# Kernel tuning notes

Measured on AMD Instinct MI355X. Metric: run time of the kernel, lower is better.

The kernel has to match this reference:

```python
import jax, jax.numpy as jnp
import numpy as np
import math


def setup_inputs() -> dict:
    key = jax.random.key(0)
    k1, k2 = jax.random.split(key)
    B, C, H, W = 16, 128, 56, 56
    Cw, ks = 16, 3  # grouped dynamic weights: groups = C // Cw = 8
    x = jax.random.normal(k1, (B, C, H, W), dtype=jnp.float32)
    w = jax.random.normal(k2, (B, Cw, ks * ks, H, W), dtype=jnp.float32)
    return {"x": x, "w": w}


def reference(x, w):
    # x: [B, C, H, W]; w: [B, Cw, ks*ks, H, W] (5-D path of SKA.forward)
    B, C, H, W = x.shape
    ks_sq = w.shape[2]
    ks = int(math.isqrt(ks_sq))
    pad = (ks - 1) // 2
    Cw = w.shape[1]
    if Cw != C:
        # torch w.repeat(1, groups, 1, 1, 1) tiles along the channel dim
        w = jnp.tile(w, (1, C // Cw, 1, 1, 1))
    # Fused equivalent of unfold * w -> sum over kernel taps: accumulate
    # shifted views of the padded input weighted by per-pixel kernels.
    xp = jnp.pad(x, ((0, 0), (0, 0), (pad, pad), (pad, pad)))
    out = jnp.zeros_like(x)
    for i in range(ks):
        for j in range(ks):
            # F.unfold flattens taps row-major: k = i * ks + j
            out = out + xp[:, :, i:i + H, j:j + W] * w[:, :, i * ks + j]
    return out
```

## Files before the change

kernel.cpp:

```cpp
#include <hip/hip_runtime.h>


#define SKA_B   16
#define SKA_C   128
#define SKA_CW  16
#define SKA_H   56
#define SKA_W   56
#define SKA_HW  (SKA_H * SKA_W)
#define SKA_G   (SKA_C / SKA_CW)

__global__ __launch_bounds__(256) void ska_kernel(
    const float* __restrict__ x,
    const float* __restrict__ w,
    float* __restrict__ out)
{
    const int tid = blockIdx.x * blockDim.x + threadIdx.x;
    const int hw  = tid % SKA_HW;
    const int bcw = tid / SKA_HW;
    const int cw  = bcw % SKA_CW;
    const int b   = bcw / SKA_CW;
    if (b >= SKA_B) return;

    const int h  = hw / SKA_W;
    const int ww = hw - h * SKA_W;

    const float* wp = w + ((size_t)(b * SKA_CW + cw) * 9) * SKA_HW + hw;
    float wk[9];
#pragma unroll
    for (int k = 0; k < 9; ++k) wk[k] = wp[(size_t)k * SKA_HW];

    const bool hv0 = (h - 1) >= 0;
    const bool hv2 = (h + 1) < SKA_H;
    const bool wv0 = (ww - 1) >= 0;
    const bool wv2 = (ww + 1) < SKA_W;

    const float* xb = x   + ((size_t)b * SKA_C + cw) * SKA_HW;
    float*       ob = out + ((size_t)b * SKA_C + cw) * SKA_HW + hw;

#pragma unroll
    for (int g = 0; g < SKA_G; ++g) {
        const float* xc = xb + (size_t)g * SKA_CW * SKA_HW + hw;
        float acc = 0.0f;

        if (hv0) {
            if (wv0) acc += xc[-SKA_W - 1] * wk[0];
                     acc += xc[-SKA_W    ] * wk[1];
            if (wv2) acc += xc[-SKA_W + 1] * wk[2];
        }
        {
            if (wv0) acc += xc[-1] * wk[3];
                     acc += xc[ 0] * wk[4];
            if (wv2) acc += xc[ 1] * wk[5];
        }
        if (hv2) {
            if (wv0) acc += xc[SKA_W - 1] * wk[6];
                     acc += xc[SKA_W    ] * wk[7];
            if (wv2) acc += xc[SKA_W + 1] * wk[8];
        }

        ob[(size_t)g * SKA_CW * SKA_HW] = acc;
    }
}

extern "C" void kernel_launch(void* const* d_in, const int* in_sizes, int n_in,
                              void* d_out, int out_size, void* d_ws, size_t ws_size,
                              hipStream_t stream) {
    const float* x = (const float*)d_in[0];
    const float* w = (const float*)d_in[1];
    float* out = (float*)d_out;

    const int total_threads = SKA_B * SKA_CW * SKA_HW;
    const int block = 256;
    const int grid = (total_threads + block - 1) / block;

    ska_kernel<<<grid, block, 0, stream>>>(x, w, out);
}
```

Before: 128.7 us.

## Compute four adjacent output columns per thread with float4 loads and stores

Each thread now produces four consecutive output pixels in a row. Weights, input rows and outputs move through 128-bit float4 accesses, and horizontally neighbouring input values are shared across the four outputs instead of being loaded again. This is meant to cut the number of memory instructions and redundant loads in a memory-bound stencil. In exchange the grid shrinks by four times and each thread uses more registers, and the row boundaries need scalar edge loads. The grid size relies on the total thread count dividing evenly by 256, and it does (200704 threads = 784 blocks).

```diff
diff --git a/kernel.cpp b/kernel.cpp
--- a/kernel.cpp
+++ b/kernel.cpp
@@ -8,57 +8,62 @@
 #define SKA_W   56
 #define SKA_HW  (SKA_H * SKA_W)
 #define SKA_G   (SKA_C / SKA_CW)
+#define SKA_Q   (SKA_W / 4)
 
 __global__ __launch_bounds__(256) void ska_kernel(
     const float* __restrict__ x,
     const float* __restrict__ w,
     float* __restrict__ out)
 {
-    const int tid = blockIdx.x * blockDim.x + threadIdx.x;
-    const int hw  = tid % SKA_HW;
-    const int bcw = tid / SKA_HW;
-    const int cw  = bcw % SKA_CW;
-    const int b   = bcw / SKA_CW;
-    if (b >= SKA_B) return;
+    const int tid = blockIdx.x * 256 + threadIdx.x;
+    const int q  = tid % SKA_Q;
+    int t        = tid / SKA_Q;
+    const int h  = t % SKA_H;
+    t            = t / SKA_H;
+    const int cw = t % SKA_CW;
+    const int b  = t / SKA_CW;
 
-    const int h  = hw / SKA_W;
-    const int ww = hw - h * SKA_W;
+    const int col = q * 4;
+    const int hw  = h * SKA_W + col;
 
     const float* wp = w + ((size_t)(b * SKA_CW + cw) * 9) * SKA_HW + hw;
-    float wk[9];
+    float4 wk[9];
 #pragma unroll
-    for (int k = 0; k < 9; ++k) wk[k] = wp[(size_t)k * SKA_HW];
+    for (int k = 0; k < 9; ++k) wk[k] = *(const float4*)(wp + (size_t)k * SKA_HW);
 
-    const bool hv0 = (h - 1) >= 0;
-    const bool hv2 = (h + 1) < SKA_H;
-    const bool wv0 = (ww - 1) >= 0;
-    const bool wv2 = (ww + 1) < SKA_W;
+    const bool hv0 = (h > 0);
+    const bool hv2 = (h < SKA_H - 1);
+    const bool lv  = (q > 0);
+    const bool rv  = (q < SKA_Q - 1);
 
-    const float* xb = x   + ((size_t)b * SKA_C + cw) * SKA_HW;
+    const float* xb = x   + ((size_t)b * SKA_C + cw) * SKA_HW + hw;
     float*       ob = out + ((size_t)b * SKA_C + cw) * SKA_HW + hw;
 
 #pragma unroll
     for (int g = 0; g < SKA_G; ++g) {
-        const float* xc = xb + (size_t)g * SKA_CW * SKA_HW + hw;
-        float acc = 0.0f;
+        const float* xc = xb + (size_t)g * SKA_CW * SKA_HW;
+        float acc0 = 0.f, acc1 = 0.f, acc2 = 0.f, acc3 = 0.f;
 
-        if (hv0) {
-            if (wv0) acc += xc[-SKA_W - 1] * wk[0];
-                     acc += xc[-SKA_W    ] * wk[1];
-            if (wv2) acc += xc[-SKA_W + 1] * wk[2];
-        }
-        {
-            if (wv0) acc += xc[-1] * wk[3];
-                     acc += xc[ 0] * wk[4];
-            if (wv2) acc += xc[ 1] * wk[5];
-        }
-        if (hv2) {
-            if (wv0) acc += xc[SKA_W - 1] * wk[6];
-                     acc += xc[SKA_W    ] * wk[7];
-            if (wv2) acc += xc[SKA_W + 1] * wk[8];
+#pragma unroll
+        for (int r = 0; r < 3; ++r) {
+            if (r == 0 && !hv0) continue;
+            if (r == 2 && !hv2) continue;
+            const float* xr = xc + (r - 1) * SKA_W;
+            const float4 m = *(const float4*)xr;
+            const float  L = lv ? xr[-1] : 0.0f;
+            const float  R = rv ? xr[4]  : 0.0f;
+            const float4 w0 = wk[3 * r + 0];
+            const float4 w1 = wk[3 * r + 1];
+            const float4 w2 = wk[3 * r + 2];
+            acc0 += L   * w0.x + m.x * w1.x + m.y * w2.x;
+            acc1 += m.x * w0.y + m.y * w1.y + m.z * w2.y;
+            acc2 += m.y * w0.z + m.z * w1.z + m.w * w2.z;
+            acc3 += m.z * w0.w + m.w * w1.w + R   * w2.w;
         }
 
-        ob[(size_t)g * SKA_CW * SKA_HW] = acc;
+        float4 o;
+        o.x = acc0; o.y = acc1; o.z = acc2; o.w = acc3;
+        *(float4*)(ob + (size_t)g * SKA_CW * SKA_HW) = o;
     }
 }
 
@@ -69,9 +74,9 @@
     const float* w = (const float*)d_in[1];
     float* out = (float*)d_out;
 
-    const int total_threads = SKA_B * SKA_CW * SKA_HW;
+    const int total_threads = SKA_B * SKA_CW * SKA_H * SKA_Q;
     const int block = 256;
-    const int grid = (total_threads + block - 1) / block;
+    const int grid = total_threads / block;
 
     ska_kernel<<<grid, block, 0, stream>>>(x, w, out);
 }
```

Result: faster. 106.9 us (-17.0%).

## Restructure SKA into row-strip sliding window with float4 loads and lane shuffles

Applied to the files above, without the earlier changes.

Each thread now computes four adjacent output columns and walks down a 14-row strip. It keeps three input rows in registers as a sliding window and gets the left and right halo values from neighbouring lanes with shuffles. Loads and stores are vectorised to float4, and stores are nontemporal. Each block covers 8 channel groups by giving them different wave segments, so every group reloads the shared dynamic weights from cache. The aim is fewer redundant global loads and fewer scalar memory instructions. In exchange there are idle lanes (14 of 16 active), a small grid of 1024 blocks of 128 threads, and serial dependence along rows.

```diff
diff --git a/kernel.cpp b/kernel.cpp
--- a/kernel.cpp
+++ b/kernel.cpp
@@ -7,58 +7,82 @@
 #define SKA_H   56
 #define SKA_W   56
 #define SKA_HW  (SKA_H * SKA_W)
-#define SKA_G   (SKA_C / SKA_CW)
+#define NSTRIP  4
+#define SROWS   14
 
-__global__ __launch_bounds__(256) void ska_kernel(
+typedef float f32x4 __attribute__((ext_vector_type(4)));
+
+__global__ __launch_bounds__(128) void ska_kernel(
     const float* __restrict__ x,
     const float* __restrict__ w,
     float* __restrict__ out)
 {
-    const int tid = blockIdx.x * blockDim.x + threadIdx.x;
-    const int hw  = tid % SKA_HW;
-    const int bcw = tid / SKA_HW;
-    const int cw  = bcw % SKA_CW;
-    const int b   = bcw / SKA_CW;
-    if (b >= SKA_B) return;
+    const int tid = threadIdx.x;
+    const int q   = tid & 15;
+    const int ch  = tid >> 4;
+    if (q >= 14) return;
 
-    const int h  = hw / SKA_W;
-    const int ww = hw - h * SKA_W;
+    const int blk   = blockIdx.x;
+    const int strip = blk & 3;
+    const int cw    = (blk >> 2) & 15;
+    const int b     = blk >> 6;
+    const int h0    = strip * SROWS;
+    const int col   = q * 4;
 
-    const float* wp = w + ((size_t)(b * SKA_CW + cw) * 9) * SKA_HW + hw;
-    float wk[9];
+    const float* xc = x   + ((size_t)b * SKA_C + ch * SKA_CW + cw) * SKA_HW + col;
+    const float* wc = w   + ((size_t)(b * SKA_CW + cw) * 9) * SKA_HW + col;
+    float*       oc = out + ((size_t)b * SKA_C + ch * SKA_CW + cw) * SKA_HW + col;
+
+    const bool ql = (q > 0);
+    const bool qr = (q < 13);
+
+    auto loadrow = [&](int h, float4& m, float& l, float& r) {
+        float4 v;
+        if (h >= 0 && h < SKA_H) {
+            v = *(const float4*)(xc + h * SKA_W);
+        } else {
+            v = make_float4(0.f, 0.f, 0.f, 0.f);
+        }
+        l = __shfl_up(v.w, 1);
+        r = __shfl_down(v.x, 1);
+        if (!ql) l = 0.f;
+        if (!qr) r = 0.f;
+        m = v;
+    };
+
+    float4 Tm, Mm, Bm;
+    float  Tl, Tr, Ml, Mr, Bl, Br;
+    loadrow(h0 - 1, Tm, Tl, Tr);
+    loadrow(h0,     Mm, Ml, Mr);
+
+#pragma unroll 2
+    for (int hh = 0; hh < SROWS; ++hh) {
+        const int h = h0 + hh;
+        loadrow(h + 1, Bm, Bl, Br);
+
+        float4 wk[9];
 #pragma unroll
-    for (int k = 0; k < 9; ++k) wk[k] = wp[(size_t)k * SKA_HW];
+        for (int k = 0; k < 9; ++k)
+            wk[k] = *(const float4*)(wc + (size_t)k * SKA_HW + h * SKA_W);
 
-    const bool hv0 = (h - 1) >= 0;
-    const bool hv2 = (h + 1) < SKA_H;
-    const bool wv0 = (ww - 1) >= 0;
-    const bool wv2 = (ww + 1) < SKA_W;
+        float a0 = Tl   * wk[0].x + Tm.x * wk[1].x + Tm.y * wk[2].x
+                 + Ml   * wk[3].x + Mm.x * wk[4].x + Mm.y * wk[5].x
+                 + Bl   * wk[6].x + Bm.x * wk[7].x + Bm.y * wk[8].x;
+        float a1 = Tm.x * wk[0].y + Tm.y * wk[1].y + Tm.z * wk[2].y
+                 + Mm.x * wk[3].y + Mm.y * wk[4].y + Mm.z * wk[5].y
+                 + Bm.x * wk[6].y + Bm.y * wk[7].y + Bm.z * wk[8].y;
+        float a2 = Tm.y * wk[0].z + Tm.z * wk[1].z + Tm.w * wk[2].z
+                 + Mm.y * wk[3].z + Mm.z * wk[4].z + Mm.w * wk[5].z
+                 + Bm.y * wk[6].z + Bm.z * wk[7].z + Bm.w * wk[8].z;
+        float a3 = Tm.z * wk[0].w + Tm.w * wk[1].w + Tr   * wk[2].w
+                 + Mm.z * wk[3].w + Mm.w * wk[4].w + Mr   * wk[5].w
+                 + Bm.z * wk[6].w + Bm.w * wk[7].w + Br   * wk[8].w;
 
-    const float* xb = x   + ((size_t)b * SKA_C + cw) * SKA_HW;
-    float*       ob = out + ((size_t)b * SKA_C + cw) * SKA_HW + hw;
+        f32x4 o = {a0, a1, a2, a3};
+        __builtin_nontemporal_store(o, (f32x4*)(oc + h * SKA_W));
 
-#pragma unroll
-    for (int g = 0; g < SKA_G; ++g) {
-        const float* xc = xb + (size_t)g * SKA_CW * SKA_HW + hw;
-        float acc = 0.0f;
-
-        if (hv0) {
-            if (wv0) acc += xc[-SKA_W - 1] * wk[0];
-                     acc += xc[-SKA_W    ] * wk[1];
-            if (wv2) acc += xc[-SKA_W + 1] * wk[2];
-        }
-        {
-            if (wv0) acc += xc[-1] * wk[3];
-                     acc += xc[ 0] * wk[4];
-            if (wv2) acc += xc[ 1] * wk[5];
-        }
-        if (hv2) {
-            if (wv0) acc += xc[SKA_W - 1] * wk[6];
-                     acc += xc[SKA_W    ] * wk[7];
-            if (wv2) acc += xc[SKA_W + 1] * wk[8];
-        }
-
-        ob[(size_t)g * SKA_CW * SKA_HW] = acc;
+        Tm = Mm; Tl = Ml; Tr = Mr;
+        Mm = Bm; Ml = Bl; Mr = Br;
     }
 }
 
@@ -69,9 +93,6 @@
     const float* w = (const float*)d_in[1];
     float* out = (float*)d_out;
 
-    const int total_threads = SKA_B * SKA_CW * SKA_HW;
-    const int block = 256;
-    const int grid = (total_threads + block - 1) / block;
-
-    ska_kernel<<<grid, block, 0, stream>>>(x, w, out);
+    const int grid = SKA_B * SKA_CW * NSTRIP;
+    ska_kernel<<<grid, 128, 0, stream>>>(x, w, out);
 }
```

Result: faster. 106.4 us (-17.3%).
